# Kernel optimization log

Hardware: AMD Instinct MI355X
Metric: run time of the kernel (lower is better)

The kernel has to match this reference:

```python
import jax, jax.numpy as jnp
import numpy as np

CODEBOOK_BITS = 8      # log2(256)
NUM_Q = 2              # NUM_QUANTIZERS
INV_TEMP = 100.0       # LFQ default inv_temperature
DIVERSITY_GAMMA = 1.0
ENTROPY_WEIGHT = 0.1   # LFQ default entropy_loss_weight
COMMIT_WEIGHT = 1.0


def conv2d(x, w, b, pad):
    out = jax.lax.conv_general_dilated(
        x, w, (1, 1), [(pad, pad), (pad, pad)],
        dimension_numbers=('NCHW', 'OIHW', 'NCHW'))
    return out + b[None, :, None, None]


def maxpool2(x):
    return jax.lax.reduce_window(x, -jnp.inf, jax.lax.max,
                                 (1, 1, 2, 2), (1, 1, 2, 2), 'VALID')


def groupnorm(x, groups=4, eps=1e-5):
    B, C, H, W = x.shape
    xg = x.reshape(B, groups, C // groups, H, W)
    mu = xg.mean(axis=(2, 3, 4), keepdims=True)
    var = xg.var(axis=(2, 3, 4), keepdims=True)
    return ((xg - mu) * jax.lax.rsqrt(var + eps)).reshape(B, C, H, W)


def upsample2(x):  # nearest, scale 2
    return jnp.repeat(jnp.repeat(x, 2, axis=2), 2, axis=3)


def lfq_codebook():
    # all 2^8 sign patterns, code j has bit i = ((j>>i)&1)*2-1
    j = jnp.arange(2 ** CODEBOOK_BITS)
    bits = ((j[:, None] >> jnp.arange(CODEBOOK_BITS)[None, :]) & 1).astype(jnp.float32)
    return bits * 2.0 - 1.0  # [256, 8]


def lfq_residual(z):
    # z: (B, D, H, W) with D = CODEBOOK_BITS
    codebook = lfq_codebook()
    t = jnp.transpose(z, (0, 2, 3, 1))  # (B,H,W,D) tokens
    residual = t
    quantized_out = jnp.zeros_like(t)
    pow2 = (2 ** jnp.arange(CODEBOOK_BITS)).astype(jnp.int32)
    indices = []
    aux = jnp.zeros((), t.dtype)
    for _ in range(NUM_Q):
        q_hard = jnp.where(residual > 0, 1.0, -1.0).astype(t.dtype)
        # straight-through binarization
        q = residual + jax.lax.stop_gradient(q_hard - residual)
        idx = jnp.sum((q_hard > 0).astype(jnp.int32) * pow2, axis=-1)  # (B,H,W)
        logits = (2.0 * INV_TEMP) * jnp.einsum('bhwd,cd->bhwc', residual, codebook)
        logp = jax.nn.log_softmax(logits, axis=-1)
        probs = jnp.exp(logp)
        per_sample_entropy = -jnp.mean(jnp.sum(probs * logp, axis=-1))
        avg_prob = jnp.mean(probs.reshape(-1, probs.shape[-1]), axis=0)
        codebook_entropy = -jnp.sum(avg_prob * jnp.log(avg_prob + 1e-10))
        entropy_aux = per_sample_entropy - DIVERSITY_GAMMA * codebook_entropy
        commit = jnp.mean((residual - jax.lax.stop_gradient(q_hard)) ** 2)
        aux = aux + ENTROPY_WEIGHT * entropy_aux + COMMIT_WEIGHT * commit
        quantized_out = quantized_out + q
        residual = residual - jax.lax.stop_gradient(q)
        indices.append(idx)
    q_out = jnp.transpose(quantized_out, (0, 3, 1, 2))  # (B,D,H,W)
    return q_out, jnp.stack(indices, axis=-1), aux


def setup_inputs() -> dict:
    key = jax.random.key(0)
    ks = jax.random.split(key, 13)
    s = 0.05
    return {
        'x': jax.random.normal(ks[0], (32, 1, 256, 256), jnp.float32),
        'w1': jax.random.normal(ks[1], (16, 1, 3, 3), jnp.float32) * s,
        'b1': jax.random.normal(ks[2], (16,), jnp.float32) * s,
        'w2': jax.random.normal(ks[3], (32, 16, 3, 3), jnp.float32) * s,
        'b2': jax.random.normal(ks[4], (32,), jnp.float32) * s,
        'w3': jax.random.normal(ks[5], (8, 32, 1, 1), jnp.float32) * s,
        'b3': jax.random.normal(ks[6], (8,), jnp.float32) * s,
        'd1': jax.random.normal(ks[7], (32, 8, 3, 3), jnp.float32) * s,
        'db1': jax.random.normal(ks[8], (32,), jnp.float32) * s,
        'd2': jax.random.normal(ks[9], (16, 32, 3, 3), jnp.float32) * s,
        'db2': jax.random.normal(ks[10], (16,), jnp.float32) * s,
        'd3': jax.random.normal(ks[11], (1, 16, 3, 3), jnp.float32) * s,
        'db3': jax.random.normal(ks[12], (1,), jnp.float32) * s,
    }


def reference(x, w1, b1, w2, b2, w3, b3, d1, db1, d2, db2, d3, db3):
    # encode
    h = jax.nn.gelu(maxpool2(conv2d(x, w1, b1, pad=1)), approximate=False)
    h = groupnorm(maxpool2(conv2d(h, w2, b2, pad=1)))
    h = conv2d(h, w3, b3, pad=0)  # (B,8,64,64)
    # residual LFQ
    q, indices, aux = lfq_residual(h)
    # decode
    y = upsample2(conv2d(q, d1, db1, pad=1))
    y = upsample2(jax.nn.gelu(conv2d(y, d2, db2, pad=1), approximate=False))
    y = conv2d(y, d3, db3, pad=1)
    return jnp.clip(y, -1.0, 1.0), indices, aux
```

## Files before the change

kernel.cpp:

```cpp
#include <hip/hip_runtime.h>
#include <hip/hip_bf16.h>
#include <math.h>

#define DEV __device__ __forceinline__

DEV float gelu_exact(float x){ return 0.5f*x*(1.0f + erff(x*0.70710678118654752f)); }

__global__ __launch_bounds__(256) void k_conv1(const float* __restrict__ x,
    const float* __restrict__ w1, const float* __restrict__ b1,
    float* __restrict__ h1,
    const float* __restrict__ w2, const float* __restrict__ d2,
    float* __restrict__ w2t, float* __restrict__ wp4d2)
{
  __shared__ float sE[34*19], sO[34*19];
  const int b = blockIdx.z;
  const int r0 = blockIdx.x*32, c0 = blockIdx.y*32;
  const float* xp = x + (size_t)b*65536;
  for(int i=threadIdx.x;i<34*34;i+=256){
    int r=i/34, c=i-r*34;
    int gr=r0+r-1, gc=c0+c-1;
    float v=0.f;
    if(gr>=0 && gr<256 && gc>=0 && gc<256) v = xp[gr*256+gc];
    if(c&1) sO[r*19+(c>>1)]=v; else sE[r*19+(c>>1)]=v;
  }
  __syncthreads();
  const int tx=threadIdx.x&15, ty=threadIdx.x>>4;
  const int base = 2*ty*19 + tx;
  float in[4][4];
  #pragma unroll
  for(int r=0;r<4;r++){
    in[r][0]=sE[base+r*19]; in[r][1]=sO[base+r*19];
    in[r][2]=sE[base+r*19+1]; in[r][3]=sO[base+r*19+1];
  }
  const int py = blockIdx.x*16+ty, px = blockIdx.y*16+tx;
  float* op = h1 + ((size_t)b*16)*16384 + py*128 + px;
  #pragma unroll
  for(int ch=0;ch<16;ch++){
    float m=-1e30f;
    #pragma unroll
    for(int pr=0;pr<2;pr++)
      #pragma unroll
      for(int pc=0;pc<2;pc++){
        float a=0.f;
        #pragma unroll
        for(int ky=0;ky<3;ky++)
          #pragma unroll
          for(int kx=0;kx<3;kx++)
            a = fmaf(in[pr+ky][pc+kx], w1[ch*9+ky*3+kx], a);
        m = fmaxf(m,a);
      }
    op[(size_t)ch*16384] = gelu_exact(m + b1[ch]);
  }
  if(blockIdx.x==0 && blockIdx.y==0 && b<8){
    const int gid = b*256 + threadIdx.x;
    for(int i=gid;i<4608;i+=2048){
      int oc=i/144, rem=i-oc*144, ic=rem/9, k=rem-ic*9;
      w2t[(ic*32+oc)*9+k]=w2[i];
    }
    for(int i=gid;i<2048;i+=2048){
      int par=i>>9, ic=(i>>4)&31, oc=i&15;
      int pyp=par>>1, pxp=par&1;
      const float* wg = d2 + ((size_t)oc*32+ic)*9;
      float a00=0.f,a01=0.f,a10=0.f,a11=0.f;
      #pragma unroll
      for(int ky=0;ky<3;ky++){
        int sy = pyp ? (ky>>1) : ((ky>0)?1:0);
        #pragma unroll
        for(int kx=0;kx<3;kx++){
          int sx = pxp ? (kx>>1) : ((kx>0)?1:0);
          float wv=wg[ky*3+kx];
          if(sy==0){ if(sx==0)a00+=wv; else a01+=wv; }
          else     { if(sx==0)a10+=wv; else a11+=wv; }
        }
      }
      float* dst=wp4d2+(size_t)i*4;
      dst[0]=a00; dst[1]=a01; dst[2]=a10; dst[3]=a11;
    }
  }
}

__global__ __launch_bounds__(256) void k_conv2(const float* __restrict__ h1,
    const float* __restrict__ w2t, const float* __restrict__ b2,
    float* __restrict__ h2, double* __restrict__ pb)
{
  __shared__ __align__(16) float t2[2][8*360];
  const int b=blockIdx.z;
  const int r0=blockIdx.x*16, c0=blockIdx.y*16;
  const float* hp = h1 + (size_t)b*16*16384;
  const int t=threadIdx.x;
  int lofs[6]; int gof[6]; bool ok0[6], ok1[6];
  #pragma unroll
  for(int s=0;s<6;s++){
    int idx=s*256+t;
    int ic=idx/162, rem=idx-162*ic, lr=rem/9, jp=rem-9*lr;
    int gr=r0+lr-1, gc=c0+2*jp-1;
    bool rok = (gr>=0) && (gr<128);
    ok0[s] = rok && (gc>=0);
    ok1[s] = rok && (gc+1<128);
    lofs[s]= ic*360+lr*20+2*jp;
    gof[s] = ic*16384 + gr*128 + gc;
  }
  float a0[6], a1[6], c0r[6], c1r[6];
  #pragma unroll
  for(int s=0;s<6;s++){
    if(s<5 || t<16){
      a0[s] = ok0[s] ? hp[gof[s]]   : 0.f;
      a1[s] = ok1[s] ? hp[gof[s]+1] : 0.f;
    }
  }
  #pragma unroll
  for(int s=0;s<6;s++)
    if(s<5 || t<16) *(float2*)&t2[0][lofs[s]]=make_float2(a0[s],a1[s]);
  const float* hp1 = hp + 8*16384;
  #pragma unroll
  for(int s=0;s<6;s++){
    if(s<5 || t<16){
      c0r[s] = ok0[s] ? hp1[gof[s]]   : 0.f;
      c1r[s] = ok1[s] ? hp1[gof[s]+1] : 0.f;
    }
  }
  __syncthreads();

  const int pos=t&63;
  const int ocg=__builtin_amdgcn_readfirstlane((int)(t>>6));
  const int oc0=ocg*8;
  const int pyl=pos>>3, pxl=pos&7;
  const int base0 = 2*pyl*20 + 2*pxl;
  float acc[8][4];
  #pragma unroll
  for(int o=0;o<8;o++)
    #pragma unroll
    for(int j=0;j<4;j++) acc[o][j]=0.f;

  #pragma unroll 4
  for(int ic=0;ic<8;ic++){
    float in[4][4];
    #pragma unroll
    for(int r=0;r<4;r++){
      float2 a=*(const float2*)&t2[0][ic*360 + base0 + r*20];
      float2 c=*(const float2*)&t2[0][ic*360 + base0 + r*20 + 2];
      in[r][0]=a.x; in[r][1]=a.y; in[r][2]=c.x; in[r][3]=c.y;
    }
    const float* wp = w2t + (ic*32+oc0)*9;
    #pragma unroll
    for(int o=0;o<8;o++){
      #pragma unroll
      for(int pr=0;pr<2;pr++)
        #pragma unroll
        for(int pc=0;pc<2;pc++){
          float s=acc[o][pr*2+pc];
          #pragma unroll
          for(int ky=0;ky<3;ky++)
            #pragma unroll
            for(int kx=0;kx<3;kx++)
              s=fmaf(in[pr+ky][pc+kx], wp[o*9+ky*3+kx], s);
          acc[o][pr*2+pc]=s;
        }
    }
  }
  #pragma unroll
  for(int s=0;s<6;s++)
    if(s<5 || t<16) *(float2*)&t2[1][lofs[s]]=make_float2(c0r[s],c1r[s]);
  __syncthreads();
  #pragma unroll 4
  for(int ic=0;ic<8;ic++){
    float in[4][4];
    #pragma unroll
    for(int r=0;r<4;r++){
      float2 a=*(const float2*)&t2[1][ic*360 + base0 + r*20];
      float2 c=*(const float2*)&t2[1][ic*360 + base0 + r*20 + 2];
      in[r][0]=a.x; in[r][1]=a.y; in[r][2]=c.x; in[r][3]=c.y;
    }
    const float* wp = w2t + ((8+ic)*32+oc0)*9;
    #pragma unroll
    for(int o=0;o<8;o++){
      #pragma unroll
      for(int pr=0;pr<2;pr++)
        #pragma unroll
        for(int pc=0;pc<2;pc++){
          float s=acc[o][pr*2+pc];
          #pragma unroll
          for(int ky=0;ky<3;ky++)
            #pragma unroll
            for(int kx=0;kx<3;kx++)
              s=fmaf(in[pr+ky][pc+kx], wp[o*9+ky*3+kx], s);
          acc[o][pr*2+pc]=s;
        }
    }
  }

  const int py=blockIdx.x*8+pyl, px=blockIdx.y*8+pxl;
  double s=0.0, s2=0.0;
  #pragma unroll
  for(int o=0;o<8;o++){
    const int oc=oc0+o;
    float m=fmaxf(fmaxf(acc[o][0],acc[o][1]),fmaxf(acc[o][2],acc[o][3]));
    float hv=m+b2[oc];
    h2[(((size_t)b*32+oc)*64+py)*64+px]=hv;
    s += (double)hv; s2 += (double)hv*(double)hv;
  }
  #pragma unroll
  for(int off=32;off;off>>=1){
    s  += __shfl_xor(s,  off, 64);
    s2 += __shfl_xor(s2, off, 64);
  }
  if(pos==0){
    const int bidx = blockIdx.x*8 + blockIdx.y;
    double* p = pb + (((size_t)b*4+ocg)*64 + bidx)*2;
    p[0]=s; p[1]=s2;
  }
}

__global__ __launch_bounds__(64) void k_stats2(const double* __restrict__ pb,
                                               float* __restrict__ stats)
{
  const int bg=blockIdx.x, t=threadIdx.x;
  double s = pb[((size_t)bg*64+t)*2], s2 = pb[((size_t)bg*64+t)*2+1];
  #pragma unroll
  for(int off=32;off;off>>=1){
    s  += __shfl_xor(s,  off, 64);
    s2 += __shfl_xor(s2, off, 64);
  }
  if(t==0){
    double mu=s/32768.0;
    double var=s2/32768.0 - mu*mu;
    stats[bg]=(float)mu;
    stats[128+bg]=(float)(1.0/sqrt(var+1e-5));
  }
}

__global__ __launch_bounds__(256) void k_lfq(const float* __restrict__ h2,
    const float* __restrict__ stats, const float* __restrict__ w3, const float* __restrict__ b3,
    float* __restrict__ qout, float* __restrict__ idxout,
    float* __restrict__ avgp, float* __restrict__ ec)
{
  __shared__ __align__(16) float tabL[16*260];
  __shared__ __align__(16) float tabH[16*260];
  const int blk=blockIdx.x;
  const int b=blk>>4;
  const int t=threadIdx.x;
  const int h=(blk&15)*4 + (t>>6);
  const int w=t&63;
  float mu[4], rs[4];
  #pragma unroll
  for(int g=0;g<4;g++){ mu[g]=stats[b*4+g]; rs[g]=stats[128+b*4+g]; }
  const float* hp = h2 + (size_t)b*131072 + h*64 + w;
  float z[8];
  #pragma unroll
  for(int d=0;d<8;d++) z[d]=b3[d];
  #pragma unroll
  for(int c=0;c<32;c++){
    float xn=(hp[(size_t)c*4096]-mu[c>>3])*rs[c>>3];
    #pragma unroll
    for(int d=0;d<8;d++) z[d]=fmaf(xn, w3[d*32+c], z[d]);
  }
  float r[8], qsum[8];
  #pragma unroll
  for(int d=0;d<8;d++){ r[d]=z[d]; qsum[d]=0.f; }
  float entk[2], comk[2];
  #pragma unroll
  for(int k=0;k<2;k++){
    int idx=0; float ent=0.f, com=0.f;
    float pb0[8], pb1[8];
    #pragma unroll
    for(int d=0;d<8;d++){
      float rv=r[d];
      bool pos = rv>0.f;
      float sgn = pos?1.f:-1.f;
      idx |= (pos?1:0)<<d;
      float dd=rv-sgn; com=fmaf(dd,dd,com);
      float a=400.f*fabsf(rv);
      float e=__expf(-a);
      float p=1.f/(1.f+e);
      ent += a - p*a - __logf(p);
      float pm=p, pq=1.f-p;
      pb1[d]=pos?pm:pq;
      pb0[d]=pos?pq:pm;
      qsum[d]+=sgn;
      r[d]=rv-sgn;
    }
    float lo[16], hi[16];
    lo[0]=pb0[0]; lo[1]=pb1[0];
    lo[2]=lo[0]*pb1[1]; lo[3]=lo[1]*pb1[1]; lo[0]*=pb0[1]; lo[1]*=pb0[1];
    lo[4]=lo[0]*pb1[2]; lo[5]=lo[1]*pb1[2]; lo[6]=lo[2]*pb1[2]; lo[7]=lo[3]*pb1[2];
    lo[0]*=pb0[2]; lo[1]*=pb0[2]; lo[2]*=pb0[2]; lo[3]*=pb0[2];
    lo[8]=lo[0]*pb1[3]; lo[9]=lo[1]*pb1[3]; lo[10]=lo[2]*pb1[3]; lo[11]=lo[3]*pb1[3];
    lo[12]=lo[4]*pb1[3]; lo[13]=lo[5]*pb1[3]; lo[14]=lo[6]*pb1[3]; lo[15]=lo[7]*pb1[3];
    lo[0]*=pb0[3]; lo[1]*=pb0[3]; lo[2]*=pb0[3]; lo[3]*=pb0[3];
    lo[4]*=pb0[3]; lo[5]*=pb0[3]; lo[6]*=pb0[3]; lo[7]*=pb0[3];
    hi[0]=pb0[4]; hi[1]=pb1[4];
    hi[2]=hi[0]*pb1[5]; hi[3]=hi[1]*pb1[5]; hi[0]*=pb0[5]; hi[1]*=pb0[5];
    hi[4]=hi[0]*pb1[6]; hi[5]=hi[1]*pb1[6]; hi[6]=hi[2]*pb1[6]; hi[7]=hi[3]*pb1[6];
    hi[0]*=pb0[6]; hi[1]*=pb0[6]; hi[2]*=pb0[6]; hi[3]*=pb0[6];
    hi[8]=hi[0]*pb1[7]; hi[9]=hi[1]*pb1[7]; hi[10]=hi[2]*pb1[7]; hi[11]=hi[3]*pb1[7];
    hi[12]=hi[4]*pb1[7]; hi[13]=hi[5]*pb1[7]; hi[14]=hi[6]*pb1[7]; hi[15]=hi[7]*pb1[7];
    hi[0]*=pb0[7]; hi[1]*=pb0[7]; hi[2]*=pb0[7]; hi[3]*=pb0[7];
    hi[4]*=pb0[7]; hi[5]*=pb0[7]; hi[6]*=pb0[7]; hi[7]*=pb0[7];
    #pragma unroll
    for(int m=0;m<16;m++){ tabL[m*260+t]=lo[m]; tabH[m*260+t]=hi[m]; }
    __syncthreads();
    float accp=0.f, accq=0.f;
    const int jl=t&15, jh=t>>4;
    const float* Lp=&tabL[jl*260];
    const float* Hp=&tabH[jh*260];
    #pragma unroll 4
    for(int q4=0;q4<64;q4++){
      float4 L=*(const float4*)&Lp[4*q4];
      float4 H=*(const float4*)&Hp[4*q4];
      accp=fmaf(L.x,H.x,accp); accq=fmaf(L.y,H.y,accq);
      accp=fmaf(L.z,H.z,accp); accq=fmaf(L.w,H.w,accq);
    }
    avgp[((size_t)k*512+blk)*256+t]=accp+accq;
    __syncthreads();
    entk[k]=ent; comk[k]=com;
    idxout[((size_t)(b*64+h)*64+w)*2+k]=(float)idx;
  }
  #pragma unroll
  for(int d=0;d<8;d++)
    qout[(((size_t)b*8+d)*64+h)*64+w]=qsum[d];
  tabL[t]=entk[0]; tabL[256+t]=entk[1]; tabL[512+t]=comk[0]; tabL[768+t]=comk[1];
  __syncthreads();
  for(int st=128;st>0;st>>=1){
    if(t<st){ tabL[t]+=tabL[t+st]; tabL[256+t]+=tabL[256+t+st];
              tabL[512+t]+=tabL[512+t+st]; tabL[768+t]+=tabL[768+t+st]; }
    __syncthreads();
  }
  if(t==0){ ec[blk*4+0]=tabL[0]; ec[blk*4+1]=tabL[256]; ec[blk*4+2]=tabL[512]; ec[blk*4+3]=tabL[768]; }
}

__global__ __launch_bounds__(256) void k_red(const float* __restrict__ avgp,
    float* __restrict__ avgs)
{
  const int k=blockIdx.x>>4, c0=(blockIdx.x&15)*16;
  const int col=threadIdx.x&15, rg=threadIdx.x>>4;
  float s=0.f;
  for(int j=0;j<32;j++){
    int blk=rg+16*j;
    s+=avgp[((size_t)k*512+blk)*256+c0+col];
  }
  __shared__ float red[256];
  red[threadIdx.x]=s; __syncthreads();
  for(int st=128;st>=16;st>>=1){
    if(threadIdx.x<st) red[threadIdx.x]+=red[threadIdx.x+st];
    __syncthreads();
  }
  if(threadIdx.x<16) avgs[k*256+c0+threadIdx.x]=red[threadIdx.x];
}

__global__ __launch_bounds__(256) void k_final(const float* __restrict__ avgs,
    const float* __restrict__ ec, float* __restrict__ auxout)
{
  __shared__ double red[256];
  const int t=threadIdx.x;
  double cb=0.0;
  #pragma unroll
  for(int k=0;k<2;k++){
    double ap=(double)avgs[k*256+t]*(1.0/131072.0);
    cb += -(ap*log(ap+1e-10));
  }
  red[t]=cb; __syncthreads();
  for(int st=128;st>0;st>>=1){ if(t<st) red[t]+=red[t+st]; __syncthreads(); }
  double CB=red[0]; __syncthreads();
  double e=0.0,c=0.0;
  for(int blk=t;blk<512;blk+=256){
    e += (double)ec[blk*4+0]+(double)ec[blk*4+1];
    c += (double)ec[blk*4+2]+(double)ec[blk*4+3];
  }
  red[t]=e; __syncthreads();
  for(int st=128;st>0;st>>=1){ if(t<st) red[t]+=red[t+st]; __syncthreads(); }
  double E=red[0]; __syncthreads();
  red[t]=c; __syncthreads();
  for(int st=128;st>0;st>>=1){ if(t<st) red[t]+=red[t+st]; __syncthreads(); }
  if(t==0){
    double C=red[0];
    double aux = 0.1*(E*(1.0/131072.0) - CB) + C*(1.0/1048576.0);
    auxout[0]=(float)aux;
  }
}

__global__ __launch_bounds__(256) void k_dec1(const float* __restrict__ q,
    const float* __restrict__ d1, const float* __restrict__ db1, float* __restrict__ out1)
{
  __shared__ float tile[8*110];
  const int b=blockIdx.z, r0=blockIdx.x*8, c0=blockIdx.y*8;
  const float* qp = q + (size_t)b*8*4096;
  for(int i=threadIdx.x;i<800;i+=256){
    int ic=i/100, rem=i-ic*100, r=rem/10, c=rem-r*10;
    int gr=r0+r-1, gc=c0+c-1;
    float v=0.f;
    if(gr>=0&&gr<64&&gc>=0&&gc<64) v=qp[ic*4096+gr*64+gc];
    tile[ic*110+r*11+c]=v;
  }
  __syncthreads();
  const int ocg=__builtin_amdgcn_readfirstlane((int)(threadIdx.x>>6));
  const int oc0=ocg*8;
  const int l=threadIdx.x&63, ry=l>>3, cx=l&7;
  float acc[8];
  #pragma unroll
  for(int o=0;o<8;o++) acc[o]=db1[oc0+o];
  #pragma unroll 2
  for(int ic=0;ic<8;ic++){
    float v[9];
    #pragma unroll
    for(int ky=0;ky<3;ky++)
      #pragma unroll
      for(int kx=0;kx<3;kx++)
        v[ky*3+kx]=tile[ic*110+(ry+ky)*11+cx+kx];
    #pragma unroll
    for(int o=0;o<8;o++){
      const float* wp=&d1[((oc0+o)*8+ic)*9];
      float s=acc[o];
      #pragma unroll
      for(int kk=0;kk<9;kk++) s=fmaf(v[kk],wp[kk],s);
      acc[o]=s;
    }
  }
  #pragma unroll
  for(int o=0;o<8;o++)
    out1[(((size_t)b*32+oc0+o)*64 + r0+ry)*64 + c0+cx]=acc[o];
}

__global__ __launch_bounds__(256) void k_dec2(const float* __restrict__ out1,
    const float* __restrict__ wp4d2, const float* __restrict__ db2, float* __restrict__ out2)
{
  __shared__ float tile[32*110];
  const int b=blockIdx.z, y0=blockIdx.x*16, x0=blockIdx.y*16;
  const int sy0=(y0>>1)-1, sx0=(x0>>1)-1;
  const float* sp = out1 + (size_t)b*32*4096;
  for(int i=threadIdx.x;i<3200;i+=256){
    int ic=i/100, rem=i-ic*100, r=rem/10, c=rem-r*10;
    int gr=sy0+r, gc=sx0+c;
    float v=0.f;
    if(gr>=0&&gr<64&&gc>=0&&gc<64) v=sp[ic*4096+gr*64+gc];
    tile[ic*110+r*11+c]=v;
  }
  __syncthreads();
  const int par=__builtin_amdgcn_readfirstlane((int)(threadIdx.x>>6));
  const int py=par>>1, px=par&1;
  const int l=threadIdx.x&63, ry=l>>3, cx=l&7;
  const int byl=ry+py, bxl=cx+px;
  float acc[16];
  #pragma unroll
  for(int o=0;o<16;o++) acc[o]=db2[o];
  #pragma unroll 2
  for(int ic=0;ic<32;ic++){
    const float* tp=&tile[ic*110 + byl*11 + bxl];
    const float s00=tp[0], s01=tp[1], s10=tp[11], s11=tp[12];
    const float* wq = wp4d2 + (size_t)((par*32+ic)*16)*4;
    #pragma unroll
    for(int o=0;o<16;o++)
      acc[o]=fmaf(s00,wq[o*4],fmaf(s01,wq[o*4+1],fmaf(s10,wq[o*4+2],fmaf(s11,wq[o*4+3],acc[o]))));
  }
  const int Y=y0+2*ry+py, X=x0+2*cx+px;
  #pragma unroll
  for(int o=0;o<16;o++)
    out2[((size_t)b*16+o)*16384 + (size_t)Y*128 + X] = gelu_exact(acc[o]);
}

__global__ __launch_bounds__(256) void k_dec3(const float* __restrict__ out2,
    const float* __restrict__ d3, const float* __restrict__ db3, float* __restrict__ y)
{
  __shared__ float tile[16*342];
  __shared__ float4 wp4[64];
  const int b=blockIdx.z, y0=blockIdx.x*32, x0=blockIdx.y*32;
  const int sy0=(y0>>1)-1, sx0=(x0>>1)-1;
  const float* sp = out2 + (size_t)b*16*16384;
  for(int i=threadIdx.x;i<16*324;i+=256){
    int ic=i/324, rem=i-ic*324, r=rem/18, c=rem-r*18;
    int gr=sy0+r, gc=sx0+c;
    float v=0.f;
    if(gr>=0&&gr<128&&gc>=0&&gc<128) v=sp[ic*16384+gr*128+gc];
    tile[ic*342+r*19+c]=v;
  }
  if(threadIdx.x<64){
    int par=threadIdx.x>>4, ic=threadIdx.x&15;
    int py=par>>1, px=par&1;
    const float* wg = d3 + ic*9;
    float a00=0.f,a01=0.f,a10=0.f,a11=0.f;
    #pragma unroll
    for(int ky=0;ky<3;ky++){
      int sy = py ? (ky>>1) : ((ky>0)?1:0);
      #pragma unroll
      for(int kx=0;kx<3;kx++){
        int sx = px ? (kx>>1) : ((kx>0)?1:0);
        float wv=wg[ky*3+kx];
        if(sy==0){ if(sx==0)a00+=wv; else a01+=wv; }
        else     { if(sx==0)a10+=wv; else a11+=wv; }
      }
    }
    wp4[threadIdx.x]=make_float4(a00,a01,a10,a11);
  }
  __syncthreads();
  const float bias=db3[0];
  const int par=__builtin_amdgcn_readfirstlane((int)(threadIdx.x>>6));
  const int py=par>>1, px=par&1;
  const int l=threadIdx.x&63, r0l=l>>4, cl=l&15;
  const int bxl=cl+px;
  float acc[4];
  #pragma unroll
  for(int a=0;a<4;a++) acc[a]=bias;
  #pragma unroll 2
  for(int ic=0;ic<16;ic++){
    const float4 wv=wp4[par*16+ic];
    #pragma unroll
    for(int a=0;a<4;a++){
      const int byl=r0l+4*a+py;
      const float* tp=&tile[ic*342 + byl*19 + bxl];
      acc[a]=fmaf(tp[0],wv.x,fmaf(tp[1],wv.y,fmaf(tp[19],wv.z,fmaf(tp[20],wv.w,acc[a]))));
    }
  }
  #pragma unroll
  for(int a=0;a<4;a++){
    const int yy=2*(r0l+4*a)+py, xx=2*cl+px;
    float v=fminf(fmaxf(acc[a],-1.0f),1.0f);
    y[(size_t)b*65536 + (size_t)(y0+yy)*256 + (x0+xx)] = v;
  }
}

extern "C" void kernel_launch(void* const* d_in, const int* in_sizes, int n_in,
                              void* d_out, int out_size, void* d_ws, size_t ws_size,
                              hipStream_t stream)
{
  const float* x  =(const float*)d_in[0];
  const float* w1 =(const float*)d_in[1];
  const float* b1 =(const float*)d_in[2];
  const float* w2 =(const float*)d_in[3];
  const float* b2 =(const float*)d_in[4];
  const float* w3 =(const float*)d_in[5];
  const float* b3 =(const float*)d_in[6];
  const float* d1 =(const float*)d_in[7];
  const float* db1=(const float*)d_in[8];
  const float* d2 =(const float*)d_in[9];
  const float* db2=(const float*)d_in[10];
  const float* d3 =(const float*)d_in[11];
  const float* db3=(const float*)d_in[12];
  float* out=(float*)d_out;
  float* ws =(float*)d_ws;
  float* h1   = ws;
  float* h2   = ws + 8388608;
  float* qb   = ws + 12582912;
  float* st   = ws + 13631488;
  float* avgp = ws + 13631744;
  float* ec   = ws + 13893888;
  float* w2t  = avgp;
  float* wp4d2= ws + 13895936;
  float* avgs = ws + 13904128;
  double* pb  = (double*)qb;
  float* out1 = h2;
  float* out2 = h1;

  k_conv1 <<<dim3(8,8,32),256,0,stream>>>(x,w1,b1,h1,w2,d2,w2t,wp4d2);
  k_conv2 <<<dim3(8,8,32),256,0,stream>>>(h1,w2t,b2,h2,pb);
  k_stats2<<<dim3(128),64,0,stream>>>(pb,st);
  k_lfq   <<<dim3(512),256,0,stream>>>(h2,st,w3,b3,qb,out+2097152,avgp,ec);
  k_red   <<<dim3(32),256,0,stream>>>(avgp,avgs);
  k_final <<<dim3(1),256,0,stream>>>(avgs,ec,out+2359296);
  k_dec1  <<<dim3(8,8,32),256,0,stream>>>(qb,d1,db1,out1);
  k_dec2  <<<dim3(8,8,32),256,0,stream>>>(out1,wp4d2,db2,out2);
  k_dec3  <<<dim3(8,8,32),256,0,stream>>>(out2,d3,db3,out);
}
```

Baseline: 192.2 us.

## Pad weights to float4, load via VMEM, fold stats and reduction kernels

Weights for conv2 and dec1 are repacked with a stride of 12 so each 3x3 filter loads as three float4 vector loads. An inline-asm zero offset makes the compiler treat those loads as per-thread vector-memory loads rather than scalar loads. dec2 also switches to float4 weight loads with a larger unroll. The GroupNorm stats kernel is folded into k_lfq, and the two aux reduction kernels become one 512-thread kernel, cutting launches at the cost of a long serial loop in a single block. Scratch buffers now live in the output tensor before it is overwritten.

```diff
diff --git a/kernel.cpp b/kernel.cpp
--- a/kernel.cpp
+++ b/kernel.cpp
@@ -5,12 +5,18 @@
 #define DEV __device__ __forceinline__
 
 DEV float gelu_exact(float x){ return 0.5f*x*(1.0f + erff(x*0.70710678118654752f)); }
+
+DEV const float* vmem_alias(const float* p){
+  int lz; asm volatile("v_mov_b32 %0, 0" : "=v"(lz));
+  return p + lz;
+}
 
 __global__ __launch_bounds__(256) void k_conv1(const float* __restrict__ x,
     const float* __restrict__ w1, const float* __restrict__ b1,
     float* __restrict__ h1,
     const float* __restrict__ w2, const float* __restrict__ d2,
-    float* __restrict__ w2t, float* __restrict__ wp4d2)
+    const float* __restrict__ d1,
+    float* __restrict__ w2p, float* __restrict__ wp4d2, float* __restrict__ d1p)
 {
   __shared__ float sE[34*19], sO[34*19];
   const int b = blockIdx.z;
@@ -55,7 +61,11 @@
     const int gid = b*256 + threadIdx.x;
     for(int i=gid;i<4608;i+=2048){
       int oc=i/144, rem=i-oc*144, ic=rem/9, k=rem-ic*9;
-      w2t[(ic*32+oc)*9+k]=w2[i];
+      w2p[(ic*32+oc)*12+k]=w2[i];
+    }
+    for(int i=gid;i<2304;i+=2048){
+      int oi=i/9, k=i-oi*9;
+      d1p[oi*12+k]=d1[i];
     }
     for(int i=gid;i<2048;i+=2048){
       int par=i>>9, ic=(i>>4)&31, oc=i&15;
@@ -80,7 +90,7 @@
 }
 
 __global__ __launch_bounds__(256) void k_conv2(const float* __restrict__ h1,
-    const float* __restrict__ w2t, const float* __restrict__ b2,
+    const float* __restrict__ w2p, const float* __restrict__ b2,
     float* __restrict__ h2, double* __restrict__ pb)
 {
   __shared__ __align__(16) float t2[2][8*360];
@@ -88,6 +98,7 @@
   const int r0=blockIdx.x*16, c0=blockIdx.y*16;
   const float* hp = h1 + (size_t)b*16*16384;
   const int t=threadIdx.x;
+  const float* wb = vmem_alias(w2p);
   int lofs[6]; int gof[6]; bool ok0[6], ok1[6];
   #pragma unroll
   for(int s=0;s<6;s++){
@@ -141,9 +152,11 @@
       float2 c=*(const float2*)&t2[0][ic*360 + base0 + r*20 + 2];
       in[r][0]=a.x; in[r][1]=a.y; in[r][2]=c.x; in[r][3]=c.y;
     }
-    const float* wp = w2t + (ic*32+oc0)*9;
     #pragma unroll
     for(int o=0;o<8;o++){
+      const float4* wp=(const float4*)(wb + (size_t)((ic*32)+oc0+o)*12);
+      float4 wA=wp[0], wB=wp[1], wC=wp[2];
+      const float wk[9]={wA.x,wA.y,wA.z,wA.w,wB.x,wB.y,wB.z,wB.w,wC.x};
       #pragma unroll
       for(int pr=0;pr<2;pr++)
         #pragma unroll
@@ -153,7 +166,7 @@
           for(int ky=0;ky<3;ky++)
             #pragma unroll
             for(int kx=0;kx<3;kx++)
-              s=fmaf(in[pr+ky][pc+kx], wp[o*9+ky*3+kx], s);
+              s=fmaf(in[pr+ky][pc+kx], wk[ky*3+kx], s);
           acc[o][pr*2+pc]=s;
         }
     }
@@ -171,9 +184,11 @@
       float2 c=*(const float2*)&t2[1][ic*360 + base0 + r*20 + 2];
       in[r][0]=a.x; in[r][1]=a.y; in[r][2]=c.x; in[r][3]=c.y;
     }
-    const float* wp = w2t + ((8+ic)*32+oc0)*9;
     #pragma unroll
     for(int o=0;o<8;o++){
+      const float4* wp=(const float4*)(wb + (size_t)(((8+ic)*32)+oc0+o)*12);
+      float4 wA=wp[0], wB=wp[1], wC=wp[2];
+      const float wk[9]={wA.x,wA.y,wA.z,wA.w,wB.x,wB.y,wB.z,wB.w,wC.x};
       #pragma unroll
       for(int pr=0;pr<2;pr++)
         #pragma unroll
@@ -183,7 +198,7 @@
           for(int ky=0;ky<3;ky++)
             #pragma unroll
             for(int kx=0;kx<3;kx++)
-              s=fmaf(in[pr+ky][pc+kx], wp[o*9+ky*3+kx], s);
+              s=fmaf(in[pr+ky][pc+kx], wk[ky*3+kx], s);
           acc[o][pr*2+pc]=s;
         }
     }
@@ -211,39 +226,39 @@
   }
 }
 
-__global__ __launch_bounds__(64) void k_stats2(const double* __restrict__ pb,
-                                               float* __restrict__ stats)
-{
-  const int bg=blockIdx.x, t=threadIdx.x;
-  double s = pb[((size_t)bg*64+t)*2], s2 = pb[((size_t)bg*64+t)*2+1];
-  #pragma unroll
-  for(int off=32;off;off>>=1){
-    s  += __shfl_xor(s,  off, 64);
-    s2 += __shfl_xor(s2, off, 64);
-  }
-  if(t==0){
-    double mu=s/32768.0;
-    double var=s2/32768.0 - mu*mu;
-    stats[bg]=(float)mu;
-    stats[128+bg]=(float)(1.0/sqrt(var+1e-5));
-  }
-}
-
 __global__ __launch_bounds__(256) void k_lfq(const float* __restrict__ h2,
-    const float* __restrict__ stats, const float* __restrict__ w3, const float* __restrict__ b3,
+    const double* __restrict__ pb, const float* __restrict__ w3, const float* __restrict__ b3,
     float* __restrict__ qout, float* __restrict__ idxout,
     float* __restrict__ avgp, float* __restrict__ ec)
 {
   __shared__ __align__(16) float tabL[16*260];
   __shared__ __align__(16) float tabH[16*260];
+  __shared__ float smu[4], srs[4];
   const int blk=blockIdx.x;
   const int b=blk>>4;
   const int t=threadIdx.x;
   const int h=(blk&15)*4 + (t>>6);
   const int w=t&63;
+  {
+    const int wv=t>>6, ln=t&63;
+    double s = pb[(((size_t)b*4+wv)*64+ln)*2];
+    double s2= pb[(((size_t)b*4+wv)*64+ln)*2+1];
+    #pragma unroll
+    for(int off=32;off;off>>=1){
+      s  += __shfl_xor(s,  off, 64);
+      s2 += __shfl_xor(s2, off, 64);
+    }
+    if(ln==0){
+      double mu=s/32768.0;
+      double var=s2/32768.0 - mu*mu;
+      smu[wv]=(float)mu;
+      srs[wv]=(float)(1.0/sqrt(var+1e-5));
+    }
+  }
+  __syncthreads();
   float mu[4], rs[4];
   #pragma unroll
-  for(int g=0;g<4;g++){ mu[g]=stats[b*4+g]; rs[g]=stats[128+b*4+g]; }
+  for(int g=0;g<4;g++){ mu[g]=smu[g]; rs[g]=srs[g]; }
   const float* hp = h2 + (size_t)b*131072 + h*64 + w;
   float z[8];
   #pragma unroll
@@ -328,62 +343,39 @@
   if(t==0){ ec[blk*4+0]=tabL[0]; ec[blk*4+1]=tabL[256]; ec[blk*4+2]=tabL[512]; ec[blk*4+3]=tabL[768]; }
 }
 
-__global__ __launch_bounds__(256) void k_red(const float* __restrict__ avgp,
-    float* __restrict__ avgs)
-{
-  const int k=blockIdx.x>>4, c0=(blockIdx.x&15)*16;
-  const int col=threadIdx.x&15, rg=threadIdx.x>>4;
+__global__ __launch_bounds__(512) void k_aux(const float* __restrict__ avgp,
+    const float* __restrict__ ec, float* __restrict__ auxout)
+{
+  __shared__ double red[512];
+  const int t=threadIdx.x;
+  const int k=t>>8, code=t&255;
   float s=0.f;
-  for(int j=0;j<32;j++){
-    int blk=rg+16*j;
-    s+=avgp[((size_t)k*512+blk)*256+c0+col];
-  }
-  __shared__ float red[256];
-  red[threadIdx.x]=s; __syncthreads();
-  for(int st=128;st>=16;st>>=1){
-    if(threadIdx.x<st) red[threadIdx.x]+=red[threadIdx.x+st];
-    __syncthreads();
-  }
-  if(threadIdx.x<16) avgs[k*256+c0+threadIdx.x]=red[threadIdx.x];
-}
-
-__global__ __launch_bounds__(256) void k_final(const float* __restrict__ avgs,
-    const float* __restrict__ ec, float* __restrict__ auxout)
-{
-  __shared__ double red[256];
-  const int t=threadIdx.x;
-  double cb=0.0;
-  #pragma unroll
-  for(int k=0;k<2;k++){
-    double ap=(double)avgs[k*256+t]*(1.0/131072.0);
-    cb += -(ap*log(ap+1e-10));
-  }
-  red[t]=cb; __syncthreads();
-  for(int st=128;st>0;st>>=1){ if(t<st) red[t]+=red[t+st]; __syncthreads(); }
+  for(int blk=0;blk<512;blk++) s += avgp[((size_t)k*512+blk)*256+code];
+  double ap=(double)s*(1.0/131072.0);
+  red[t]=-(ap*log(ap+1e-10));
+  __syncthreads();
+  for(int st=256;st>0;st>>=1){ if(t<st) red[t]+=red[t+st]; __syncthreads(); }
   double CB=red[0]; __syncthreads();
-  double e=0.0,c=0.0;
-  for(int blk=t;blk<512;blk+=256){
-    e += (double)ec[blk*4+0]+(double)ec[blk*4+1];
-    c += (double)ec[blk*4+2]+(double)ec[blk*4+3];
-  }
+  double e=(double)ec[t*4+0]+(double)ec[t*4+1];
+  double c=(double)ec[t*4+2]+(double)ec[t*4+3];
   red[t]=e; __syncthreads();
-  for(int st=128;st>0;st>>=1){ if(t<st) red[t]+=red[t+st]; __syncthreads(); }
+  for(int st=256;st>0;st>>=1){ if(t<st) red[t]+=red[t+st]; __syncthreads(); }
   double E=red[0]; __syncthreads();
   red[t]=c; __syncthreads();
-  for(int st=128;st>0;st>>=1){ if(t<st) red[t]+=red[t+st]; __syncthreads(); }
+  for(int st=256;st>0;st>>=1){ if(t<st) red[t]+=red[t+st]; __syncthreads(); }
   if(t==0){
     double C=red[0];
-    double aux = 0.1*(E*(1.0/131072.0) - CB) + C*(1.0/1048576.0);
-    auxout[0]=(float)aux;
+    auxout[0]=(float)(0.1*(E*(1.0/131072.0) - CB) + C*(1.0/1048576.0));
   }
 }
 
 __global__ __launch_bounds__(256) void k_dec1(const float* __restrict__ q,
-    const float* __restrict__ d1, const float* __restrict__ db1, float* __restrict__ out1)
+    const float* __restrict__ d1p, const float* __restrict__ db1, float* __restrict__ out1)
 {
   __shared__ float tile[8*110];
   const int b=blockIdx.z, r0=blockIdx.x*8, c0=blockIdx.y*8;
   const float* qp = q + (size_t)b*8*4096;
+  const float* wb = vmem_alias(d1p);
   for(int i=threadIdx.x;i<800;i+=256){
     int ic=i/100, rem=i-ic*100, r=rem/10, c=rem-r*10;
     int gr=r0+r-1, gc=c0+c-1;
@@ -408,10 +400,12 @@
         v[ky*3+kx]=tile[ic*110+(ry+ky)*11+cx+kx];
     #pragma unroll
     for(int o=0;o<8;o++){
-      const float* wp=&d1[((oc0+o)*8+ic)*9];
+      const float4* wp=(const float4*)(wb + (size_t)(((oc0+o)*8)+ic)*12);
+      float4 wA=wp[0], wB=wp[1], wC=wp[2];
+      const float wk[9]={wA.x,wA.y,wA.z,wA.w,wB.x,wB.y,wB.z,wB.w,wC.x};
       float s=acc[o];
       #pragma unroll
-      for(int kk=0;kk<9;kk++) s=fmaf(v[kk],wp[kk],s);
+      for(int kk=0;kk<9;kk++) s=fmaf(v[kk],wk[kk],s);
       acc[o]=s;
     }
   }
@@ -427,6 +421,7 @@
   const int b=blockIdx.z, y0=blockIdx.x*16, x0=blockIdx.y*16;
   const int sy0=(y0>>1)-1, sx0=(x0>>1)-1;
   const float* sp = out1 + (size_t)b*32*4096;
+  const float* wbf = vmem_alias(wp4d2);
   for(int i=threadIdx.x;i<3200;i+=256){
     int ic=i/100, rem=i-ic*100, r=rem/10, c=rem-r*10;
     int gr=sy0+r, gc=sx0+c;
@@ -442,14 +437,16 @@
   float acc[16];
   #pragma unroll
   for(int o=0;o<16;o++) acc[o]=db2[o];
-  #pragma unroll 2
+  #pragma unroll 4
   for(int ic=0;ic<32;ic++){
     const float* tp=&tile[ic*110 + byl*11 + bxl];
     const float s00=tp[0], s01=tp[1], s10=tp[11], s11=tp[12];
-    const float* wq = wp4d2 + (size_t)((par*32+ic)*16)*4;
-    #pragma unroll
-    for(int o=0;o<16;o++)
-      acc[o]=fmaf(s00,wq[o*4],fmaf(s01,wq[o*4+1],fmaf(s10,wq[o*4+2],fmaf(s11,wq[o*4+3],acc[o]))));
+    const float4* wq4=(const float4*)(wbf + (size_t)((par*32+ic)*16)*4);
+    #pragma unroll
+    for(int o=0;o<16;o++){
+      float4 wv=wq4[o];
+      acc[o]=fmaf(s00,wv.x,fmaf(s01,wv.y,fmaf(s10,wv.z,fmaf(s11,wv.w,acc[o]))));
+    }
   }
   const int Y=y0+2*ry+py, X=x0+2*cx+px;
   #pragma unroll
@@ -539,23 +536,20 @@
   float* h1   = ws;
   float* h2   = ws + 8388608;
   float* qb   = ws + 12582912;
-  float* st   = ws + 13631488;
   float* avgp = ws + 13631744;
   float* ec   = ws + 13893888;
-  float* w2t  = avgp;
   float* wp4d2= ws + 13895936;
-  float* avgs = ws + 13904128;
-  double* pb  = (double*)qb;
+  float* w2p  = avgp;
+  double* pb  = (double*)out;
+  float* d1p  = out + 32768;
   float* out1 = h2;
   float* out2 = h1;
 
-  k_conv1 <<<dim3(8,8,32),256,0,stream>>>(x,w1,b1,h1,w2,d2,w2t,wp4d2);
-  k_conv2 <<<dim3(8,8,32),256,0,stream>>>(h1,w2t,b2,h2,pb);
-  k_stats2<<<dim3(128),64,0,stream>>>(pb,st);
-  k_lfq   <<<dim3(512),256,0,stream>>>(h2,st,w3,b3,qb,out+2097152,avgp,ec);
-  k_red   <<<dim3(32),256,0,stream>>>(avgp,avgs);
-  k_final <<<dim3(1),256,0,stream>>>(avgs,ec,out+2359296);
-  k_dec1  <<<dim3(8,8,32),256,0,stream>>>(qb,d1,db1,out1);
-  k_dec2  <<<dim3(8,8,32),256,0,stream>>>(out1,wp4d2,db2,out2);
-  k_dec3  <<<dim3(8,8,32),256,0,stream>>>(out2,d3,db3,out);
-}
+  k_conv1<<<dim3(8,8,32),256,0,stream>>>(x,w1,b1,h1,w2,d2,d1,w2p,wp4d2,d1p);
+  k_conv2<<<dim3(8,8,32),256,0,stream>>>(h1,w2p,b2,h2,pb);
+  k_lfq  <<<dim3(512),256,0,stream>>>(h2,pb,w3,b3,qb,out+2097152,avgp,ec);
+  k_aux  <<<dim3(1),512,0,stream>>>(avgp,ec,out+2359296);
+  k_dec1 <<<dim3(8,8,32),256,0,stream>>>(qb,d1p,db1,out1);
+  k_dec2 <<<dim3(8,8,32),256,0,stream>>>(out1,wp4d2,db2,out2);
+  k_dec3 <<<dim3(8,8,32),256,0,stream>>>(out2,d3,db3,out);
+}
```

New measurement: 338.3 us. 76.0% more time.
